# Optimization experiments

Measured on AMD Instinct MI355X. Metric: run time of the kernel, lower is better.

Reference implementation:

```python
import jax, jax.numpy as jnp
import numpy as np

B = 65536       # number of segments (molecules/graphs) = max(batch_indices[0]) + 1
N = 1048576     # nodes per eye
IN_NF, R_OUT, C_OUT = 64, 128, 128
BRAIN_IN, BRAIN_H, BRAIN_OUT = 256, 256, 128


def setup_inputs() -> dict:
    key = jax.random.key(0)
    ks = jax.random.split(key, 16)
    f = jax.random.normal
    s_in = 1.0 / np.sqrt(IN_NF)
    s_r = 1.0 / np.sqrt(R_OUT)
    s_b = 1.0 / np.sqrt(BRAIN_IN)
    s_h = 1.0 / np.sqrt(BRAIN_H)
    return {
        "x0": f(ks[0], (N, IN_NF), jnp.float32),
        "x1": f(ks[1], (N, IN_NF), jnp.float32),
        "idx0": jax.random.randint(ks[2], (N,), 0, B, dtype=jnp.int32),
        "idx1": jax.random.randint(ks[3], (N,), 0, B, dtype=jnp.int32),
        "Wr0": f(ks[4], (IN_NF, R_OUT), jnp.float32) * s_in,
        "br0": jnp.zeros((R_OUT,), jnp.float32),
        "Wc0": f(ks[5], (R_OUT, C_OUT), jnp.float32) * s_r,
        "bc0": jnp.zeros((C_OUT,), jnp.float32),
        "Wr1": f(ks[6], (IN_NF, R_OUT), jnp.float32) * s_in,
        "br1": jnp.zeros((R_OUT,), jnp.float32),
        "Wc1": f(ks[7], (R_OUT, C_OUT), jnp.float32) * s_r,
        "bc1": jnp.zeros((C_OUT,), jnp.float32),
        "Wb1": f(ks[8], (BRAIN_IN, BRAIN_H), jnp.float32) * s_b,
        "bb1": jnp.zeros((BRAIN_H,), jnp.float32),
        "Wb2": f(ks[9], (BRAIN_H, BRAIN_OUT), jnp.float32) * s_h,
        "bb2": jnp.zeros((BRAIN_OUT,), jnp.float32),
    }


def _eye(x, idx, Wr, br, Wc, bc):
    # linear + relu per node: [N, r_out]
    h = jax.nn.relu(x @ Wr + br)
    # scatter-mean over segments -> [B, r_out]; empty segments get 0 (matches
    # torch_scatter mean and the original zero-padding up to maxlen)
    s = jax.ops.segment_sum(h, idx, num_segments=B)
    cnt = jax.ops.segment_sum(jnp.ones((h.shape[0],), h.dtype), idx, num_segments=B)
    mean = s / jnp.maximum(cnt, 1.0)[:, None]
    # per-graph linear + relu -> [B, c_out]
    return jax.nn.relu(mean @ Wc + bc)


def reference(x0, x1, idx0, idx1, Wr0, br0, Wc0, bc0, Wr1, br1, Wc1, bc1, Wb1, bb1, Wb2, bb2):
    e0 = _eye(x0, idx0, Wr0, br0, Wc0, bc0)   # [B, 128]
    e1 = _eye(x1, idx1, Wr1, br1, Wc1, bc1)   # [B, 128]
    z = jnp.concatenate([e0, e1], axis=1)      # [B, 256]
    h = jax.nn.relu(z @ Wb1 + bb1)             # [B, 256]
    return h @ Wb2 + bb2                       # [B, 128]
```

## Files before the change

kernel.cpp:

```cpp
#include <hip/hip_runtime.h>
#include <hip/hip_bf16.h>

#define B_SEG 65536
#define N_NODES 1048576

typedef _Float16 f16;
typedef __attribute__((ext_vector_type(8))) _Float16 f16x8;
typedef __attribute__((ext_vector_type(2))) __fp16 fp16x2;
typedef __attribute__((ext_vector_type(4))) float f32x4;
typedef unsigned short u16;

union F16x8 { f16x8 v; fp16x2 h2[4]; };

#define MFMA16(a, b, acc) __builtin_amdgcn_mfma_f32_16x16x32_f16((a), (b), (acc), 0, 0, 0)

__global__ __launch_bounds__(256) void histo_part(const int* __restrict__ idx0,
        const int* __restrict__ idx1, int* __restrict__ cnt0, int* __restrict__ cnt1,
        u16* __restrict__ rank0, u16* __restrict__ rank1) {
    int part  = blockIdx.x & 7;
    int chunk = blockIdx.x >> 3;
    int base  = chunk * (N_NODES / 256);
    for (int i = base + threadIdx.x; i < base + N_NODES / 256; i += 256) {
        int s0 = idx0[i];
        if ((s0 >> 13) == part) { int p = atomicAdd(&cnt0[s0], 1); rank0[i] = (u16)p; }
        int s1 = idx1[i];
        if ((s1 >> 13) == part) { int p = atomicAdd(&cnt1[s1], 1); rank1[i] = (u16)p; }
    }
}

__global__ __launch_bounds__(256) void scan1(const int* __restrict__ cnt, int* __restrict__ bsum) {
    int b = blockIdx.x, t = threadIdx.x;
    int4 v = ((const int4*)cnt)[b * 256 + t];
    int s = v.x + v.y + v.z + v.w;
    for (int d = 1; d < 64; d <<= 1) s += __shfl_xor(s, d);
    __shared__ int ws4[4];
    if ((t & 63) == 0) ws4[t >> 6] = s;
    __syncthreads();
    if (t == 0) bsum[b] = ws4[0] + ws4[1] + ws4[2] + ws4[3];
}

__global__ __launch_bounds__(128) void scan2(int* __restrict__ bsum) {
    int t = threadIdx.x, lane = t & 63;
    int v = bsum[t];
    int s = v;
    for (int d = 1; d < 64; d <<= 1) { int u = __shfl_up(s, d); if (lane >= d) s += u; }
    bsum[t] = s - v;
}

__global__ __launch_bounds__(256) void scan3(const int* __restrict__ cnt, const int* __restrict__ bsum,
                                             int* __restrict__ off0, int* __restrict__ off1) {
    int b = blockIdx.x, t = threadIdx.x;
    int4 v = ((const int4*)cnt)[b * 256 + t];
    int local = v.x + v.y + v.z + v.w;
    int lane = t & 63, w = t >> 6;
    int s = local;
    for (int d = 1; d < 64; d <<= 1) { int u = __shfl_up(s, d); if (lane >= d) s += u; }
    __shared__ int wsum[4];
    if (lane == 63) wsum[w] = s;
    __syncthreads();
    int carry = bsum[b];
    for (int i = 0; i < w; ++i) carry += wsum[i];
    int ex = carry + s - local;
    int* off = (b < 64) ? off0 : off1;
    int gi = (b & 63) * 1024 + t * 4;
    off[gi] = ex; ex += v.x; off[gi + 1] = ex; ex += v.y; off[gi + 2] = ex; ex += v.z; off[gi + 3] = ex;
    if (b == 0 && t == 0) { off0[B_SEG] = N_NODES; off1[B_SEG] = N_NODES; }
}

__global__ __launch_bounds__(256) void fill_simple(const int* __restrict__ idx0,
        const int* __restrict__ idx1, const u16* __restrict__ rank0, const u16* __restrict__ rank1,
        const int* __restrict__ off0, const int* __restrict__ off1,
        int* __restrict__ ord0, int* __restrict__ ord1) {
    int stride = gridDim.x * blockDim.x;
    for (int i = blockIdx.x * blockDim.x + threadIdx.x; i < N_NODES; i += stride) {
        ord0[off0[idx0[i]] + rank0[i]] = i;
        ord1[off1[idx1[i]] + rank1[i]] = i;
    }
}

__global__ __launch_bounds__(256) void prep_weights(
        const float* __restrict__ Wc0, const float* __restrict__ Wc1,
        const float* __restrict__ Wb1, const float* __restrict__ Wb2,
        f16* __restrict__ T0, f16* __restrict__ T1, f16* __restrict__ T2, f16* __restrict__ T3) {
    int b = blockIdx.x, t = threadIdx.x;
    if (b < 64)        { int i = b * 256 + t;         T0[i] = (f16)Wc0[(i & 127) * 128 + (i >> 7)]; }
    else if (b < 128)  { int i = (b - 64) * 256 + t;  T1[i] = (f16)Wc1[(i & 127) * 128 + (i >> 7)]; }
    else if (b < 384)  { int i = (b - 128) * 256 + t; T2[i] = (f16)Wb1[(i & 255) * 256 + (i >> 8)]; }
    else               { int i = (b - 384) * 256 + t; T3[i] = (f16)Wb2[(i & 255) * 128 + (i >> 8)]; }
}

#define SEGS_PER_WAVE 8
__global__ __launch_bounds__(256, 3) void eye_means_mfma(
        const float* __restrict__ xA, const float* __restrict__ WrA, const float* __restrict__ brA,
        const int* __restrict__ offA, const int* __restrict__ ordA, f16* __restrict__ meansA,
        const float* __restrict__ xB, const float* __restrict__ WrB, const float* __restrict__ brB,
        const int* __restrict__ offB, const int* __restrict__ ordB, f16* __restrict__ meansB) {
    const float *x, *Wr, *br; const int *off, *ord; f16* means;
    if (blockIdx.y == 0) { x = xA; Wr = WrA; br = brA; off = offA; ord = ordA; means = meansA; }
    else                 { x = xB; Wr = WrB; br = brB; off = offB; ord = ordB; means = meansB; }

    int lane = threadIdx.x & 63;
    int wid  = blockIdx.x * 4 + (threadIdx.x >> 6);
    int c  = lane & 15;
    int kq = lane >> 4;

    f16x8 bfr[8][2];
    float rbias[8];
    #pragma unroll
    for (int g = 0; g < 8; ++g) {
        #pragma unroll
        for (int h = 0; h < 2; ++h)
            #pragma unroll
            for (int j = 0; j < 8; ++j)
                bfr[g][h][j] = (f16)Wr[(size_t)(h * 32 + kq * 8 + j) * 128 + g * 16 + c];
        rbias[g] = br[g * 16 + c];
    }

    int s_begin = wid * SEGS_PER_WAVE;
    int offv  = off[s_begin + ((lane <= 8) ? lane : 8)];
    int base0 = __shfl(offv, 0);
    int nxtv  = __shfl(offv, (lane < 8) ? (lane + 1) : 8);
    int szl   = nxtv - offv;

    int ov0 = ord[base0 + lane];
    int ov1 = ord[base0 + 64 + lane];
    int ov2 = ord[base0 + 128 + lane];

    auto node_at = [&](int off_rel, int sz, int r) -> int {
        int e  = off_rel + r;
        int e6 = e & 63;
        int n0 = __shfl(ov0, e6);
        int n1 = __shfl(ov1, e6);
        int n2 = __shfl(ov2, e6);
        int n  = (e < 64) ? n0 : (e < 128) ? n1 : n2;
        if (e >= 192) n = ord[base0 + e];
        return (r < sz) ? n : 0;
    };

    auto loadx = [&](int node, float4& v0, float4& v1, float4& v2, float4& v3) {
        const float* xp = &x[(size_t)node * 64 + kq * 8];
        v0 = *(const float4*)(xp);      v1 = *(const float4*)(xp + 4);
        v2 = *(const float4*)(xp + 32); v3 = *(const float4*)(xp + 36);
    };

    float sum[8];
    #pragma unroll
    for (int g = 0; g < 8; ++g) sum[g] = 0.f;

    float4 ca, cb, cc, cd;
    {
        int sz0 = __shfl(szl, 0);
        loadx(node_at(0, sz0, c), ca, cb, cc, cd);
    }

    #pragma unroll
    for (int s = 0; s < SEGS_PER_WAVE; ++s) {
        int off_rel   = __shfl(offv, s) - base0;
        int sz        = __shfl(szl, s);
        int nb        = (sz + 15) >> 4;
        int off_rel_n = (s < SEGS_PER_WAVE - 1) ? (__shfl(offv, s + 1) - base0) : 0;
        int sz_n      = (s < SEGS_PER_WAVE - 1) ? __shfl(szl, s + 1) : 0;
        size_t mb     = (size_t)(s_begin + s) * 128;

        if (nb == 0) {
            means[mb + (2 * kq + 0) * 16 + c] = (f16)0.f;
            means[mb + (2 * kq + 1) * 16 + c] = (f16)0.f;
            loadx(node_at(off_rel_n, sz_n, c), ca, cb, cc, cd);
            continue;
        }

        for (int b = 0; b < nb; ++b) {
            int nn = (b + 1 < nb) ? node_at(off_rel, sz, (b + 1) * 16 + c)
                                  : node_at(off_rel_n, sz_n, c);
            float4 pa, pb, pc, pd;
            loadx(nn, pa, pb, pc, pd);

            f16x8 A0 = {}, A1 = {};
            if (b * 16 + c < sz) {
                F16x8 u0, u1;
                u0.h2[0] = __builtin_amdgcn_cvt_pkrtz(ca.x, ca.y);
                u0.h2[1] = __builtin_amdgcn_cvt_pkrtz(ca.z, ca.w);
                u0.h2[2] = __builtin_amdgcn_cvt_pkrtz(cb.x, cb.y);
                u0.h2[3] = __builtin_amdgcn_cvt_pkrtz(cb.z, cb.w);
                u1.h2[0] = __builtin_amdgcn_cvt_pkrtz(cc.x, cc.y);
                u1.h2[1] = __builtin_amdgcn_cvt_pkrtz(cc.z, cc.w);
                u1.h2[2] = __builtin_amdgcn_cvt_pkrtz(cd.x, cd.y);
                u1.h2[3] = __builtin_amdgcn_cvt_pkrtz(cd.z, cd.w);
                A0 = u0.v; A1 = u1.v;
            }
            #pragma unroll
            for (int g = 0; g < 8; ++g) {
                f32x4 acc = {0.f, 0.f, 0.f, 0.f};
                acc = MFMA16(A0, bfr[g][0], acc);
                acc = MFMA16(A1, bfr[g][1], acc);
                #pragma unroll
                for (int r = 0; r < 4; ++r)
                    sum[g] += fmaxf(acc[r] + rbias[g], 0.f);
            }
            ca = pa; cb = pb; cc = pc; cd = pd;
        }

        float padc = (float)(nb * 16 - sz);
        float inv  = 1.f / (float)sz;
        #pragma unroll
        for (int g = 0; g < 8; ++g) {
            float v = sum[g];
            v += __shfl_xor(v, 16);
            v += __shfl_xor(v, 32);
            v -= padc * fmaxf(rbias[g], 0.f);
            sum[g] = v * inv;
        }
        means[mb + (2 * kq + 0) * 16 + c] = (f16)sum[2 * kq + 0];
        means[mb + (2 * kq + 1) * 16 + c] = (f16)sum[2 * kq + 1];
        #pragma unroll
        for (int g = 0; g < 8; ++g) sum[g] = 0.f;
    }
}

template<int K, int RELU, int OUT16>
__global__ __launch_bounds__(256) void gemm16(
        const f16* __restrict__ A, const f16* __restrict__ BT,
        const float* __restrict__ bias, void* __restrict__ Cv, int ldc) {
    int lane = threadIdx.x & 63;
    int w = threadIdx.x >> 6;
    int c = lane & 15, kq = lane >> 4;
    int m0 = blockIdx.x * 128 + w * 32;
    int n0 = blockIdx.y * 128;

    f32x4 acc[2][8] = {};
    const f16* arow0 = A + (size_t)(m0 + c) * K + kq * 8;
    const f16* arow1 = arow0 + (size_t)16 * K;
    const f16* brow  = BT + (size_t)(n0 + c) * K + kq * 8;

    #pragma unroll 2
    for (int k0 = 0; k0 < K; k0 += 32) {
        f16x8 a0 = *(const f16x8*)(arow0 + k0);
        f16x8 a1 = *(const f16x8*)(arow1 + k0);
        #pragma unroll
        for (int g = 0; g < 8; ++g) {
            f16x8 bf = *(const f16x8*)(brow + (size_t)g * 16 * K + k0);
            acc[0][g] = MFMA16(a0, bf, acc[0][g]);
            acc[1][g] = MFMA16(a1, bf, acc[1][g]);
        }
    }

    #pragma unroll
    for (int g = 0; g < 8; ++g) {
        float bv = bias[n0 + g * 16 + c];
        #pragma unroll
        for (int ms = 0; ms < 2; ++ms) {
            #pragma unroll
            for (int r = 0; r < 4; ++r) {
                float v = acc[ms][g][r] + bv;
                if (RELU) v = fmaxf(v, 0.f);
                size_t ci = (size_t)(m0 + ms * 16 + kq * 4 + r) * ldc + n0 + g * 16 + c;
                if (OUT16) ((f16*)Cv)[ci] = (f16)v;
                else       ((float*)Cv)[ci] = v;
            }
        }
    }
}

__global__ __launch_bounds__(256) void gemm_wc(
        const f16* __restrict__ M0, const f16* __restrict__ M1,
        const f16* __restrict__ T0, const f16* __restrict__ T1,
        const float* __restrict__ bc0, const float* __restrict__ bc1,
        f16* __restrict__ z) {
    int e = blockIdx.y;
    const f16* A  = e ? M1 : M0;
    const f16* BT = e ? T1 : T0;
    const float* bias = e ? bc1 : bc0;
    int lane = threadIdx.x & 63;
    int w = threadIdx.x >> 6;
    int c = lane & 15, kq = lane >> 4;
    int m0 = blockIdx.x * 128 + w * 32;

    f32x4 acc[2][8] = {};
    const f16* arow0 = A + (size_t)(m0 + c) * 128 + kq * 8;
    const f16* arow1 = arow0 + (size_t)16 * 128;
    const f16* brow  = BT + (size_t)c * 128 + kq * 8;

    #pragma unroll
    for (int k0 = 0; k0 < 128; k0 += 32) {
        f16x8 a0 = *(const f16x8*)(arow0 + k0);
        f16x8 a1 = *(const f16x8*)(arow1 + k0);
        #pragma unroll
        for (int g = 0; g < 8; ++g) {
            f16x8 bf = *(const f16x8*)(brow + (size_t)g * 16 * 128 + k0);
            acc[0][g] = MFMA16(a0, bf, acc[0][g]);
            acc[1][g] = MFMA16(a1, bf, acc[1][g]);
        }
    }

    #pragma unroll
    for (int g = 0; g < 8; ++g) {
        float bv = bias[g * 16 + c];
        #pragma unroll
        for (int ms = 0; ms < 2; ++ms) {
            #pragma unroll
            for (int r = 0; r < 4; ++r) {
                float v = fmaxf(acc[ms][g][r] + bv, 0.f);
                z[(size_t)(m0 + ms * 16 + kq * 4 + r) * 256 + e * 128 + g * 16 + c] = (f16)v;
            }
        }
    }
}

extern "C" void kernel_launch(void* const* d_in, const int* in_sizes, int n_in,
                              void* d_out, int out_size, void* d_ws, size_t ws_size,
                              hipStream_t stream) {
    const float* x0  = (const float*)d_in[0];
    const float* x1  = (const float*)d_in[1];
    const int*   idx0 = (const int*)d_in[2];
    const int*   idx1 = (const int*)d_in[3];
    const float* Wr0 = (const float*)d_in[4];
    const float* br0 = (const float*)d_in[5];
    const float* Wc0 = (const float*)d_in[6];
    const float* bc0 = (const float*)d_in[7];
    const float* Wr1 = (const float*)d_in[8];
    const float* br1 = (const float*)d_in[9];
    const float* Wc1 = (const float*)d_in[10];
    const float* bc1 = (const float*)d_in[11];
    const float* Wb1 = (const float*)d_in[12];
    const float* bb1 = (const float*)d_in[13];
    const float* Wb2 = (const float*)d_in[14];
    const float* bb2 = (const float*)d_in[15];
    float* out = (float*)d_out;

    char* w = (char*)d_ws;
    auto alloc = [&](size_t bytes) { void* p = (void*)w; w += (bytes + 255) & ~(size_t)255; return p; };
    int* cnt0 = (int*)alloc((size_t)B_SEG * 4);
    int* cnt1 = (int*)alloc((size_t)B_SEG * 4);
    int* off0 = (int*)alloc((size_t)(B_SEG + 1) * 4);
    int* off1 = (int*)alloc((size_t)(B_SEG + 1) * 4);
    int* ord0 = (int*)alloc((size_t)(N_NODES + 256) * 4);
    int* ord1 = (int*)alloc((size_t)(N_NODES + 256) * 4);
    u16* rank0 = (u16*)alloc((size_t)N_NODES * 2);
    u16* rank1 = (u16*)alloc((size_t)N_NODES * 2);
    int* bsum = (int*)alloc(128 * 4);
    f16* means0 = (f16*)alloc((size_t)B_SEG * 128 * 2);
    f16* means1 = (f16*)alloc((size_t)B_SEG * 128 * 2);
    f16* z      = (f16*)alloc((size_t)B_SEG * 256 * 2);
    f16* hb     = (f16*)alloc((size_t)B_SEG * 256 * 2);
    f16* T0     = (f16*)alloc((size_t)128 * 128 * 2);
    f16* T1     = (f16*)alloc((size_t)128 * 128 * 2);
    f16* T2     = (f16*)alloc((size_t)256 * 256 * 2);
    f16* T3     = (f16*)alloc((size_t)128 * 256 * 2);

    (void)hipMemsetAsync(cnt0, 0, 2 * (size_t)B_SEG * sizeof(int), stream);
    histo_part<<<2048, 256, 0, stream>>>(idx0, idx1, cnt0, cnt1, rank0, rank1);
    scan1<<<128, 256, 0, stream>>>(cnt0, bsum);
    scan2<<<1, 128, 0, stream>>>(bsum);
    scan3<<<128, 256, 0, stream>>>(cnt0, bsum, off0, off1);
    fill_simple<<<2048, 256, 0, stream>>>(idx0, idx1, rank0, rank1, off0, off1, ord0, ord1);
    prep_weights<<<512, 256, 0, stream>>>(Wc0, Wc1, Wb1, Wb2, T0, T1, T2, T3);

    eye_means_mfma<<<dim3(2048, 2), 256, 0, stream>>>(
        x0, Wr0, br0, off0, ord0, means0,
        x1, Wr1, br1, off1, ord1, means1);

    gemm_wc<<<dim3(512, 2), 256, 0, stream>>>(means0, means1, T0, T1, bc0, bc1, z);
    gemm16<256, 1, 1><<<dim3(512, 2), 256, 0, stream>>>(z,  T2, bb1, hb,  256);
    gemm16<256, 0, 0><<<dim3(512, 1), 256, 0, stream>>>(hb, T3, bb2, out, 128);
}
```

Baseline: 421.4 us.

## Pre-convert node features to fp16 in histogram kernel, gather fp16 in eye kernel

```diff
diff --git a/kernel.cpp b/kernel.cpp
--- a/kernel.cpp
+++ b/kernel.cpp
@@ -14,17 +14,42 @@
 
 #define MFMA16(a, b, acc) __builtin_amdgcn_mfma_f32_16x16x32_f16((a), (b), (acc), 0, 0, 0)
 
-__global__ __launch_bounds__(256) void histo_part(const int* __restrict__ idx0,
-        const int* __restrict__ idx1, int* __restrict__ cnt0, int* __restrict__ cnt1,
+__global__ __launch_bounds__(256) void conv_histo(
+        const float* __restrict__ x0, const float* __restrict__ x1,
+        f16* __restrict__ xh0, f16* __restrict__ xh1,
+        const int* __restrict__ idx0, const int* __restrict__ idx1,
+        int* __restrict__ cnt0, int* __restrict__ cnt1,
         u16* __restrict__ rank0, u16* __restrict__ rank1) {
-    int part  = blockIdx.x & 7;
-    int chunk = blockIdx.x >> 3;
-    int base  = chunk * (N_NODES / 256);
-    for (int i = base + threadIdx.x; i < base + N_NODES / 256; i += 256) {
-        int s0 = idx0[i];
-        if ((s0 >> 13) == part) { int p = atomicAdd(&cnt0[s0], 1); rank0[i] = (u16)p; }
-        int s1 = idx1[i];
-        if ((s1 >> 13) == part) { int p = atomicAdd(&cnt1[s1], 1); rank1[i] = (u16)p; }
+    if (blockIdx.x < 2048) {
+        int part  = blockIdx.x & 7;
+        int chunk = blockIdx.x >> 3;
+        int base  = chunk * (N_NODES / 256);
+        for (int i = base + threadIdx.x; i < base + N_NODES / 256; i += 256) {
+            int s0 = idx0[i];
+            if ((s0 >> 13) == part) { int p = atomicAdd(&cnt0[s0], 1); rank0[i] = (u16)p; }
+            int s1 = idx1[i];
+            if ((s1 >> 13) == part) { int p = atomicAdd(&cnt1[s1], 1); rank1[i] = (u16)p; }
+        }
+    } else {
+        const int stride = 2048 * 256;
+        int tid = (blockIdx.x - 2048) * 256 + threadIdx.x;
+        const int ngroups = N_NODES * 64 / 8;
+        for (int j = tid; j < ngroups; j += stride) {
+            float4 a0 = ((const float4*)x0)[j * 2], b0 = ((const float4*)x0)[j * 2 + 1];
+            F16x8 u0;
+            u0.h2[0] = __builtin_amdgcn_cvt_pkrtz(a0.x, a0.y);
+            u0.h2[1] = __builtin_amdgcn_cvt_pkrtz(a0.z, a0.w);
+            u0.h2[2] = __builtin_amdgcn_cvt_pkrtz(b0.x, b0.y);
+            u0.h2[3] = __builtin_amdgcn_cvt_pkrtz(b0.z, b0.w);
+            ((f16x8*)xh0)[j] = u0.v;
+            float4 a1 = ((const float4*)x1)[j * 2], b1 = ((const float4*)x1)[j * 2 + 1];
+            F16x8 u1;
+            u1.h2[0] = __builtin_amdgcn_cvt_pkrtz(a1.x, a1.y);
+            u1.h2[1] = __builtin_amdgcn_cvt_pkrtz(a1.z, a1.w);
+            u1.h2[2] = __builtin_amdgcn_cvt_pkrtz(b1.x, b1.y);
+            u1.h2[3] = __builtin_amdgcn_cvt_pkrtz(b1.z, b1.w);
+            ((f16x8*)xh1)[j] = u1.v;
+        }
     }
 }
 
@@ -91,11 +116,11 @@
 
 #define SEGS_PER_WAVE 8
 __global__ __launch_bounds__(256, 3) void eye_means_mfma(
-        const float* __restrict__ xA, const float* __restrict__ WrA, const float* __restrict__ brA,
+        const f16* __restrict__ xA, const float* __restrict__ WrA, const float* __restrict__ brA,
         const int* __restrict__ offA, const int* __restrict__ ordA, f16* __restrict__ meansA,
-        const float* __restrict__ xB, const float* __restrict__ WrB, const float* __restrict__ brB,
+        const f16* __restrict__ xB, const float* __restrict__ WrB, const float* __restrict__ brB,
         const int* __restrict__ offB, const int* __restrict__ ordB, f16* __restrict__ meansB) {
-    const float *x, *Wr, *br; const int *off, *ord; f16* means;
+    const f16 *x; const float *Wr, *br; const int *off, *ord; f16* means;
     if (blockIdx.y == 0) { x = xA; Wr = WrA; br = brA; off = offA; ord = ordA; means = meansA; }
     else                 { x = xB; Wr = WrB; br = brB; off = offB; ord = ordB; means = meansB; }
 
@@ -137,20 +162,22 @@
         return (r < sz) ? n : 0;
     };
 
-    auto loadx = [&](int node, float4& v0, float4& v1, float4& v2, float4& v3) {
-        const float* xp = &x[(size_t)node * 64 + kq * 8];
-        v0 = *(const float4*)(xp);      v1 = *(const float4*)(xp + 4);
-        v2 = *(const float4*)(xp + 32); v3 = *(const float4*)(xp + 36);
+    auto loadx = [&](int node, f16x8& B0, f16x8& B1) {
+        const f16* xp = &x[(size_t)node * 64 + kq * 8];
+        B0 = *(const f16x8*)(xp);
+        B1 = *(const f16x8*)(xp + 32);
     };
 
     float sum[8];
     #pragma unroll
     for (int g = 0; g < 8; ++g) sum[g] = 0.f;
 
-    float4 ca, cb, cc, cd;
+    const f16x8 zf = {};
+
+    f16x8 ca, cb;
     {
         int sz0 = __shfl(szl, 0);
-        loadx(node_at(0, sz0, c), ca, cb, cc, cd);
+        loadx(node_at(0, sz0, c), ca, cb);
     }
 
     #pragma unroll
@@ -165,29 +192,19 @@
         if (nb == 0) {
             means[mb + (2 * kq + 0) * 16 + c] = (f16)0.f;
             means[mb + (2 * kq + 1) * 16 + c] = (f16)0.f;
-            loadx(node_at(off_rel_n, sz_n, c), ca, cb, cc, cd);
+            loadx(node_at(off_rel_n, sz_n, c), ca, cb);
             continue;
         }
 
         for (int b = 0; b < nb; ++b) {
             int nn = (b + 1 < nb) ? node_at(off_rel, sz, (b + 1) * 16 + c)
                                   : node_at(off_rel_n, sz_n, c);
-            float4 pa, pb, pc, pd;
-            loadx(nn, pa, pb, pc, pd);
-
-            f16x8 A0 = {}, A1 = {};
-            if (b * 16 + c < sz) {
-                F16x8 u0, u1;
-                u0.h2[0] = __builtin_amdgcn_cvt_pkrtz(ca.x, ca.y);
-                u0.h2[1] = __builtin_amdgcn_cvt_pkrtz(ca.z, ca.w);
-                u0.h2[2] = __builtin_amdgcn_cvt_pkrtz(cb.x, cb.y);
-                u0.h2[3] = __builtin_amdgcn_cvt_pkrtz(cb.z, cb.w);
-                u1.h2[0] = __builtin_amdgcn_cvt_pkrtz(cc.x, cc.y);
-                u1.h2[1] = __builtin_amdgcn_cvt_pkrtz(cc.z, cc.w);
-                u1.h2[2] = __builtin_amdgcn_cvt_pkrtz(cd.x, cd.y);
-                u1.h2[3] = __builtin_amdgcn_cvt_pkrtz(cd.z, cd.w);
-                A0 = u0.v; A1 = u1.v;
-            }
+            f16x8 pa, pb;
+            loadx(nn, pa, pb);
+
+            bool valid = (b * 16 + c < sz);
+            f16x8 A0 = valid ? ca : zf;
+            f16x8 A1 = valid ? cb : zf;
             #pragma unroll
             for (int g = 0; g < 8; ++g) {
                 f32x4 acc = {0.f, 0.f, 0.f, 0.f};
@@ -197,7 +214,7 @@
                 for (int r = 0; r < 4; ++r)
                     sum[g] += fmaxf(acc[r] + rbias[g], 0.f);
             }
-            ca = pa; cb = pb; cc = pc; cd = pd;
+            ca = pa; cb = pb;
         }
 
         float padc = (float)(nb * 16 - sz);
@@ -329,6 +346,8 @@
 
     char* w = (char*)d_ws;
     auto alloc = [&](size_t bytes) { void* p = (void*)w; w += (bytes + 255) & ~(size_t)255; return p; };
+    f16* xh0 = (f16*)alloc((size_t)N_NODES * 64 * 2);
+    f16* xh1 = (f16*)alloc((size_t)N_NODES * 64 * 2);
     int* cnt0 = (int*)alloc((size_t)B_SEG * 4);
     int* cnt1 = (int*)alloc((size_t)B_SEG * 4);
     int* off0 = (int*)alloc((size_t)(B_SEG + 1) * 4);
@@ -348,7 +367,8 @@
     f16* T3     = (f16*)alloc((size_t)128 * 256 * 2);
 
     (void)hipMemsetAsync(cnt0, 0, 2 * (size_t)B_SEG * sizeof(int), stream);
-    histo_part<<<2048, 256, 0, stream>>>(idx0, idx1, cnt0, cnt1, rank0, rank1);
+    conv_histo<<<4096, 256, 0, stream>>>(x0, x1, xh0, xh1, idx0, idx1,
+                                         cnt0, cnt1, rank0, rank1);
     scan1<<<128, 256, 0, stream>>>(cnt0, bsum);
     scan2<<<1, 128, 0, stream>>>(bsum);
     scan3<<<128, 256, 0, stream>>>(cnt0, bsum, off0, off1);
@@ -356,8 +376,8 @@
     prep_weights<<<512, 256, 0, stream>>>(Wc0, Wc1, Wb1, Wb2, T0, T1, T2, T3);
 
     eye_means_mfma<<<dim3(2048, 2), 256, 0, stream>>>(
-        x0, Wr0, br0, off0, ord0, means0,
-        x1, Wr1, br1, off1, ord1, means1);
+        xh0, Wr0, br0, off0, ord0, means0,
+        xh1, Wr1, br1, off1, ord1, means1);
 
     gemm_wc<<<dim3(512, 2), 256, 0, stream>>>(means0, means1, T0, T1, bc0, bc1, z);
     gemm16<256, 1, 1><<<dim3(512, 2), 256, 0, stream>>>(z,  T2, bb1, hb,  256);
```

After: 521.7 us. 23.8% more time.
